# Kernel tuning notes

Hardware: AMD Instinct MI355X
Metric: run time of the kernel (lower is better)

Reference implementation:

```python
import jax, jax.numpy as jnp
import numpy as np

EPS = 1e-05
KEEP_RATIO = 0.7


def setup_inputs() -> dict:
    key = jax.random.key(0)
    ks = jax.random.split(key, 10)
    B, C, L, H = 8, 512, 8192, 128
    return {
        "x": jax.random.normal(ks[0], (B, C, L), dtype=jnp.float32),
        "c": jax.random.normal(ks[1], (B, C, L), dtype=jnp.float32),
        "gw1": jax.random.normal(ks[2], (H, C), dtype=jnp.float32) * 0.05,
        "gb1": jax.random.normal(ks[3], (H,), dtype=jnp.float32) * 0.05,
        "gw2": jax.random.normal(ks[4], (C, H), dtype=jnp.float32) * 0.05,
        "gb2": jax.random.normal(ks[5], (C,), dtype=jnp.float32) * 0.05,
        "mw1": jax.random.normal(ks[6], (H, C), dtype=jnp.float32) * 0.05,
        "mb1": jax.random.normal(ks[7], (H,), dtype=jnp.float32) * 0.05,
        "mw2": jax.random.normal(ks[8], (2 * C, H), dtype=jnp.float32) * 0.05,
        "mb2": jax.random.normal(ks[9], (2 * C,), dtype=jnp.float32) * 0.05,
    }


def reference(x, c, gw1, gb1, gw2, gb2, mw1, mb1, mw2, mb2):
    B, C, L = x.shape
    # per-channel stats over L
    mu_c = jnp.mean(x, axis=2, keepdims=True)                 # [B,C,1]
    var_c = jnp.var(x, axis=2, keepdims=True)                 # ddof=0
    sigma_c = jnp.sqrt(var_c + EPS)
    # per-sample stats over (C,L)
    mu_l = jnp.mean(x, axis=(1, 2), keepdims=True)            # [B,1,1]
    var_l = jnp.var(x, axis=(1, 2), keepdims=True)
    sigma_l = jnp.sqrt(var_l + EPS)
    # gate network on c (1x1 convs == channel matmuls), then mean over L
    h = jax.nn.relu(jnp.einsum('hc,bcl->bhl', gw1, c) + gb1[None, :, None])
    g = jax.nn.sigmoid(jnp.einsum('ch,bhl->bcl', gw2, h) + gb2[None, :, None])
    g_mix = jnp.mean(g, axis=2, keepdims=True)                # [B,C,1]
    mu = g_mix * mu_c + (1.0 - g_mix) * mu_l
    sigma = g_mix * sigma_c + (1.0 - g_mix) * sigma_l
    x_hat = (x - mu) / sigma
    # MLP on pooled condition -> gamma, beta
    cond_pool = jnp.mean(c, axis=2)                           # [B,C]
    hm = jax.nn.relu(jnp.einsum('hc,bc->bh', mw1, cond_pool) + mb1)
    gamma_beta = jnp.einsum('oh,bh->bo', mw2, hm) + mb2       # [B,2C]
    gamma = gamma_beta[:, :C][:, :, None]                     # [B,C,1]
    beta = gamma_beta[:, C:][:, :, None]
    y = (1.0 + gamma) * x_hat + beta
    # top-k channel mask by mean |y| over L
    imp = jnp.mean(jnp.abs(y), axis=2)                        # [B,C]
    k = max(1, int(C * KEEP_RATIO))
    _, idx = jax.lax.top_k(imp, k)                            # [B,k]
    mask = jnp.zeros((B, C), dtype=y.dtype).at[jnp.arange(B)[:, None], idx].set(1.0)
    return y * mask[:, :, None]
```

## Files before the change

kernel.cpp:

```cpp
#include <hip/hip_runtime.h>
#include <hip/hip_bf16.h>
#include <math.h>

#define NB 8
#define NC 512
#define NL 8192
#define NH 128
#define FEPS 1e-5f
#define NKEEP 358

typedef __attribute__((ext_vector_type(8))) short short8;
typedef __attribute__((ext_vector_type(4))) float f32x4;

__device__ __forceinline__ unsigned short f2bf(float x) {
  unsigned u = __float_as_uint(x);
  return (unsigned short)((u + 0x7fffu + ((u >> 16) & 1u)) >> 16);
}
__device__ __forceinline__ unsigned pack2(float a, float b) {
  return (unsigned)f2bf(a) | ((unsigned)f2bf(b) << 16);
}

__global__ __launch_bounds__(256) void k1_xstats(
    const float* __restrict__ x, float* __restrict__ xsum, float* __restrict__ xsumsq,
    const float* __restrict__ gw1, const float* __restrict__ gw2,
    unsigned short* __restrict__ gw1b, unsigned short* __restrict__ gw2b,
    float* __restrict__ csum, float* __restrict__ gsum) {
  const int bc = blockIdx.x;
  const int t = threadIdx.x;
  if (bc < 256) {
    const int i = bc * 256 + t;
    gw1b[i] = f2bf(gw1[i]);
    gw2b[i] = f2bf(gw2[i]);
    if (i < NB * NC) { csum[i] = 0.f; gsum[i] = 0.f; }
  }
  const float4* xp = reinterpret_cast<const float4*>(x + (size_t)bc * NL);
  float s1 = 0.f, s2 = 0.f;
#pragma unroll
  for (int i = 0; i < 8; ++i) {
    float4 v = xp[i * 256 + t];
    s1 += v.x + v.y + v.z + v.w;
    s2 += v.x * v.x + v.y * v.y + v.z * v.z + v.w * v.w;
  }
  for (int off = 32; off; off >>= 1) { s1 += __shfl_down(s1, off); s2 += __shfl_down(s2, off); }
  __shared__ float r1[4], r2[4];
  if ((t & 63) == 0) { r1[t >> 6] = s1; r2[t >> 6] = s2; }
  __syncthreads();
  if (t == 0) {
    xsum[bc]   = r1[0] + r1[1] + r1[2] + r1[3];
    xsumsq[bc] = r2[0] + r2[1] + r2[2] + r2[3];
  }
}

__global__ __launch_bounds__(256, 2) void k2_gate(
    const float* __restrict__ cin,
    const unsigned short* __restrict__ gw1b, const unsigned short* __restrict__ gw2b,
    const float* __restrict__ gb1, const float* __restrict__ gb2,
    float* __restrict__ gsum_g, float* __restrict__ csum_g) {
  __shared__ __align__(16) unsigned AsU[2 * 128 * 36];
  __shared__ __align__(16) unsigned short Hts[4][32][136];
  __shared__ float gsum_s[NC], csum_s[NC], gb2_s[NC];
  __shared__ float gb1_s[NH];

  const int t = threadIdx.x;
  const int lane = t & 63;
  const int w = t >> 6;
  const int r = lane & 15;
  const int kg = lane >> 4;
  const int b = blockIdx.x >> 6;
  const int l0 = (blockIdx.x & 63) * 128;

  const int p = t >> 3;
  const int q = t & 7;

  f32x4 acc0[8], acc1[8];
#pragma unroll
  for (int i = 0; i < 8; ++i) { acc0[i] = (f32x4){0.f,0.f,0.f,0.f}; acc1[i] = (f32x4){0.f,0.f,0.f,0.f}; }

  const float* cbase = cin + (size_t)b * NC * NL + l0;
  const unsigned short* gw1r = gw1b + (size_t)r * NC + kg * 8;

  f32x4 vaA[4], vbA[4], vaB[4], vbB[4];

#define LOADA(dA, dB, kch) { \
    _Pragma("unroll") \
    for (int pass = 0; pass < 4; ++pass) { \
      const float* cp0 = cbase + (size_t)((kch) * 64 + 2 * p) * NL + 32 * pass + 4 * q; \
      dA[pass] = __builtin_nontemporal_load(reinterpret_cast<const f32x4*>(cp0)); \
      dB[pass] = __builtin_nontemporal_load(reinterpret_cast<const f32x4*>(cp0 + NL)); \
    } }

#define WRITEA(sA, sB, kch, bufi) { \
    unsigned* dst = AsU + (bufi) * (128 * 36); \
    float sa = 0.f, sb = 0.f; \
    _Pragma("unroll") \
    for (int pass = 0; pass < 4; ++pass) { \
      const int ll = 32 * pass + 4 * q; \
      sa += sA[pass].x + sA[pass].y + sA[pass].z + sA[pass].w; \
      sb += sB[pass].x + sB[pass].y + sB[pass].z + sB[pass].w; \
      dst[(ll + 0) * 36 + p] = pack2(sA[pass].x, sB[pass].x); \
      dst[(ll + 1) * 36 + p] = pack2(sA[pass].y, sB[pass].y); \
      dst[(ll + 2) * 36 + p] = pack2(sA[pass].z, sB[pass].z); \
      dst[(ll + 3) * 36 + p] = pack2(sA[pass].w, sB[pass].w); \
    } \
    sa += __shfl_xor(sa, 1); sa += __shfl_xor(sa, 2); sa += __shfl_xor(sa, 4); \
    sb += __shfl_xor(sb, 1); sb += __shfl_xor(sb, 2); sb += __shfl_xor(sb, 4); \
    if ((lane & 7) == 0) { \
      atomicAdd(&csum_s[(kch) * 64 + 2 * p],     sa); \
      atomicAdd(&csum_s[(kch) * 64 + 2 * p + 1], sb); \
    } }

  LOADA(vaA, vbA, 0)
  LOADA(vaB, vbB, 1)
  for (int i = t; i < NC; i += 256) { gsum_s[i] = 0.f; csum_s[i] = 0.f; gb2_s[i] = gb2[i]; }
  if (t < NH) gb1_s[t] = gb1[t];
  __syncthreads();
  WRITEA(vaA, vbA, 0, 0)
  asm volatile("s_waitcnt lgkmcnt(0)" ::: "memory");
  __builtin_amdgcn_s_barrier();
  __builtin_amdgcn_sched_barrier(0);

  for (int k = 0; k < 8; ++k) {
    const unsigned* Abuf = AsU + (k & 1) * (128 * 36);
    short8 bfr[16];
#pragma unroll
    for (int ht = 0; ht < 8; ++ht) {
      bfr[2 * ht]     = *reinterpret_cast<const short8*>(gw1r + (size_t)(ht * 16) * NC + k * 64);
      bfr[2 * ht + 1] = *reinterpret_cast<const short8*>(gw1r + (size_t)(ht * 16) * NC + k * 64 + 32);
    }
    short8 a0[2], a1[2];
#pragma unroll
    for (int kk = 0; kk < 2; ++kk) {
      a0[kk] = *reinterpret_cast<const short8*>(&Abuf[(32 * w + r)      * 36 + 16 * kk + 4 * kg]);
      a1[kk] = *reinterpret_cast<const short8*>(&Abuf[(32 * w + 16 + r) * 36 + 16 * kk + 4 * kg]);
    }
    __builtin_amdgcn_sched_barrier(0);
    if (k < 7) {
      if ((k & 1) == 0) { WRITEA(vaB, vbB, k + 1, 1) } else { WRITEA(vaA, vbA, k + 1, 0) }
    }
    __builtin_amdgcn_sched_barrier(0);
    if (k < 6) {
      if ((k & 1) == 0) { LOADA(vaA, vbA, k + 2) } else { LOADA(vaB, vbB, k + 2) }
    }
    __builtin_amdgcn_sched_barrier(0);
#pragma unroll
    for (int kk = 0; kk < 2; ++kk) {
#pragma unroll
      for (int ht = 0; ht < 8; ++ht) {
        acc0[ht] = __builtin_amdgcn_mfma_f32_16x16x32_bf16(a0[kk], bfr[2 * ht + kk], acc0[ht], 0, 0, 0);
        acc1[ht] = __builtin_amdgcn_mfma_f32_16x16x32_bf16(a1[kk], bfr[2 * ht + kk], acc1[ht], 0, 0, 0);
      }
    }
    __builtin_amdgcn_sched_barrier(0);
    asm volatile("s_waitcnt lgkmcnt(0)" ::: "memory");
    __builtin_amdgcn_s_barrier();
    __builtin_amdgcn_sched_barrier(0);
  }

#pragma unroll
  for (int ht = 0; ht < 8; ++ht) {
    const float bias = gb1_s[16 * ht + r];
#pragma unroll
    for (int reg = 0; reg < 4; ++reg) {
      Hts[w][4 * kg + reg][16 * ht + r]      = f2bf(fmaxf(acc0[ht][reg] + bias, 0.f));
      Hts[w][16 + 4 * kg + reg][16 * ht + r] = f2bf(fmaxf(acc1[ht][reg] + bias, 0.f));
    }
  }
  short8 af0[4], af1[4];
#pragma unroll
  for (int kk = 0; kk < 4; ++kk) {
    af0[kk] = *reinterpret_cast<const short8*>(&Hts[w][r][32 * kk + 8 * kg]);
    af1[kk] = *reinterpret_cast<const short8*>(&Hts[w][16 + r][32 * kk + 8 * kg]);
  }

  unsigned short* Bs2 = reinterpret_cast<unsigned short*>(AsU);
  const int crow = lane >> 4;
  const int bs2  = lane & 15;
  short8 bv[4];

#define LOADB2(ccn) { \
    _Pragma("unroll") \
    for (int j = 0; j < 4; ++j) { \
      const int cl = 16 * w + 4 * j + crow; \
      bv[j] = *reinterpret_cast<const short8*>(gw2b + (size_t)((ccn) * 64 + cl) * NH + bs2 * 8); \
    } }
#define WRITEB2(ccn) { \
    unsigned short* dstb = Bs2 + ((ccn) & 1) * 8192; \
    _Pragma("unroll") \
    for (int j = 0; j < 4; ++j) { \
      const int cl = 16 * w + 4 * j + crow; \
      *reinterpret_cast<short8*>(&dstb[cl * 128 + ((bs2 ^ (cl & 7)) * 8)]) = bv[j]; \
    } }

  LOADB2(0)
  WRITEB2(0)
  __syncthreads();
  for (int cc = 0; cc < 8; ++cc) {
    if (cc < 7) LOADB2(cc + 1)
    const unsigned short* Bbuf = Bs2 + (cc & 1) * 8192;
#pragma unroll
    for (int ctt = 0; ctt < 4; ++ctt) {
      f32x4 z0 = (f32x4){0.f,0.f,0.f,0.f}, z1 = (f32x4){0.f,0.f,0.f,0.f};
#pragma unroll
      for (int kk = 0; kk < 4; ++kk) {
        const short8 bf = *reinterpret_cast<const short8*>(
            &Bbuf[(16 * ctt + r) * 128 + (((4 * kk + kg) ^ (r & 7)) * 8)]);
        z0 = __builtin_amdgcn_mfma_f32_16x16x32_bf16(af0[kk], bf, z0, 0, 0, 0);
        z1 = __builtin_amdgcn_mfma_f32_16x16x32_bf16(af1[kk], bf, z1, 0, 0, 0);
      }
      const float bias = gb2_s[cc * 64 + 16 * ctt + r];
      float s = 0.f;
#pragma unroll
      for (int reg = 0; reg < 4; ++reg) {
        s += 1.f / (1.f + __expf(-(z0[reg] + bias)));
        s += 1.f / (1.f + __expf(-(z1[reg] + bias)));
      }
      s += __shfl_xor(s, 16);
      s += __shfl_xor(s, 32);
      if (lane < 16) atomicAdd(&gsum_s[cc * 64 + 16 * ctt + lane], s);
    }
    if (cc < 7) WRITEB2(cc + 1)
    __syncthreads();
  }
  for (int i = t; i < NC; i += 256) {
    atomicAdd(&gsum_g[b * NC + i], gsum_s[i]);
    atomicAdd(&csum_g[b * NC + i], csum_s[i]);
  }
}

__global__ __launch_bounds__(256) void k3_final(
    const float* __restrict__ xsum, const float* __restrict__ xsumsq,
    const float* __restrict__ csum, const float* __restrict__ gsum,
    const float* __restrict__ mw1, const float* __restrict__ mb1,
    const float* __restrict__ mw2, const float* __restrict__ mb2,
    float* __restrict__ a_arr, float* __restrict__ d_arr) {
  __shared__ __align__(16) float cp[NC];
  __shared__ __align__(16) float hm[NH];
  __shared__ float gbv[2 * NC];
  __shared__ double red[8];
  __shared__ float mu_l_s, sig_l_s;
  const int b = blockIdx.x, t = threadIdx.x;

  double s1 = 0.0, s2 = 0.0;
  for (int c = t; c < NC; c += 256) { s1 += (double)xsum[b * NC + c]; s2 += (double)xsumsq[b * NC + c]; }
  for (int off = 32; off; off >>= 1) { s1 += __shfl_down(s1, off); s2 += __shfl_down(s2, off); }
  if ((t & 63) == 0) { red[(t >> 6) * 2] = s1; red[(t >> 6) * 2 + 1] = s2; }
  for (int c = t; c < NC; c += 256) cp[c] = csum[b * NC + c] * (1.f / NL);
  __syncthreads();
  if (t == 0) {
    double S1 = red[0] + red[2] + red[4] + red[6];
    double S2 = red[1] + red[3] + red[5] + red[7];
    double n = (double)NC * NL;
    double mu = S1 / n;
    double var = S2 / n - mu * mu;
    mu_l_s = (float)mu;
    sig_l_s = (float)sqrt(var + (double)FEPS);
  }
  __syncthreads();
  if (t < NH) {
    const float4* row = reinterpret_cast<const float4*>(mw1 + (size_t)t * NC);
    const float4* cpv = reinterpret_cast<const float4*>(cp);
    float acc = mb1[t];
    for (int i = 0; i < NC / 4; ++i) {
      float4 wv = row[i], xv = cpv[i];
      acc += wv.x * xv.x + wv.y * xv.y + wv.z * xv.z + wv.w * xv.w;
    }
    hm[t] = fmaxf(acc, 0.f);
  }
  __syncthreads();
  for (int o = t; o < 2 * NC; o += 256) {
    const float4* row = reinterpret_cast<const float4*>(mw2 + (size_t)o * NH);
    const float4* hv = reinterpret_cast<const float4*>(hm);
    float acc = mb2[o];
    for (int i = 0; i < NH / 4; ++i) {
      float4 wv = row[i], xv = hv[i];
      acc += wv.x * xv.x + wv.y * xv.y + wv.z * xv.z + wv.w * xv.w;
    }
    gbv[o] = acc;
  }
  __syncthreads();
  const float mu_l = mu_l_s, sig_l = sig_l_s;
  for (int c = t; c < NC; c += 256) {
    float gm = gsum[b * NC + c] * (1.f / NL);
    double mu_c = (double)xsum[b * NC + c] / NL;
    double var_c = (double)xsumsq[b * NC + c] / NL - mu_c * mu_c;
    float sig_c = (float)sqrt(var_c + (double)FEPS);
    float mu = gm * (float)mu_c + (1.f - gm) * mu_l;
    float sg = gm * sig_c + (1.f - gm) * sig_l;
    float gamma = gbv[c], beta = gbv[NC + c];
    float A = (1.f + gamma) / sg;
    a_arr[b * NC + c] = A;
    d_arr[b * NC + c] = beta - A * mu;
  }
}

__global__ __launch_bounds__(256) void k4_y(
    const float* __restrict__ x, const float* __restrict__ a_arr,
    const float* __restrict__ d_arr, float* __restrict__ out, float* __restrict__ imp) {
  const int bc = blockIdx.x, t = threadIdx.x;
  const float A = a_arr[bc], D = d_arr[bc];
  const f32x4* xp = reinterpret_cast<const f32x4*>(x + (size_t)bc * NL);
  f32x4* op = reinterpret_cast<f32x4*>(out + (size_t)bc * NL);
  float s = 0.f;
#pragma unroll
  for (int i = 0; i < 8; ++i) {
    f32x4 v = __builtin_nontemporal_load(xp + i * 256 + t);
    f32x4 y;
    y.x = fmaf(A, v.x, D); y.y = fmaf(A, v.y, D);
    y.z = fmaf(A, v.z, D); y.w = fmaf(A, v.w, D);
    s += fabsf(y.x) + fabsf(y.y) + fabsf(y.z) + fabsf(y.w);
    __builtin_nontemporal_store(y, op + i * 256 + t);
  }
  for (int off = 32; off; off >>= 1) s += __shfl_down(s, off);
  __shared__ float rs[4];
  if ((t & 63) == 0) rs[t >> 6] = s;
  __syncthreads();
  if (t == 0) imp[bc] = rs[0] + rs[1] + rs[2] + rs[3];
}

__global__ __launch_bounds__(256) void k5_apply(
    const float* __restrict__ imp, float* __restrict__ out) {
  const int bc = blockIdx.x;
  const int b = bc >> 9;
  const int c = bc & (NC - 1);
  const int t = threadIdx.x;
  const float* row = imp + b * NC;
  const float mine = row[c];
  int cnt = 0;
#pragma unroll
  for (int jj = 0; jj < 2; ++jj) {
    const int j = jj * 256 + t;
    const float o = row[j];
    cnt += (o > mine) || (o == mine && j < c);
  }
  for (int off = 32; off; off >>= 1) cnt += __shfl_down(cnt, off);
  __shared__ int rs[4];
  if ((t & 63) == 0) rs[t >> 6] = cnt;
  __syncthreads();
  const int rank = rs[0] + rs[1] + rs[2] + rs[3];
  if (rank < NKEEP) return;
  f32x4* op = reinterpret_cast<f32x4*>(out + (size_t)bc * NL);
  const f32x4 z = (f32x4){0.f, 0.f, 0.f, 0.f};
#pragma unroll
  for (int i = 0; i < 8; ++i) __builtin_nontemporal_store(z, op + i * 256 + t);
}

extern "C" void kernel_launch(void* const* d_in, const int* in_sizes, int n_in,
                              void* d_out, int out_size, void* d_ws, size_t ws_size,
                              hipStream_t stream) {
  const float* x   = (const float*)d_in[0];
  const float* c   = (const float*)d_in[1];
  const float* gw1 = (const float*)d_in[2];
  const float* gb1 = (const float*)d_in[3];
  const float* gw2 = (const float*)d_in[4];
  const float* gb2 = (const float*)d_in[5];
  const float* mw1 = (const float*)d_in[6];
  const float* mb1 = (const float*)d_in[7];
  const float* mw2 = (const float*)d_in[8];
  const float* mb2 = (const float*)d_in[9];
  float* out = (float*)d_out;
  char* ws = (char*)d_ws;

  unsigned short* gw1b = (unsigned short*)(ws);
  unsigned short* gw2b = (unsigned short*)(ws + 131072);
  float* xsum   = (float*)(ws + 262144);
  float* xsumsq = (float*)(ws + 278528);
  float* csum   = (float*)(ws + 294912);
  float* gsum   = (float*)(ws + 311296);
  float* a_arr  = (float*)(ws + 327680);
  float* d_arr  = (float*)(ws + 344064);
  float* imp    = (float*)(ws + 360448);

  k1_xstats<<<NB * NC, 256, 0, stream>>>(x, xsum, xsumsq, gw1, gw2, gw1b, gw2b, csum, gsum);
  k2_gate<<<NB * (NL / 128), 256, 0, stream>>>(c, gw1b, gw2b, gb1, gb2, gsum, csum);
  k3_final<<<NB, 256, 0, stream>>>(xsum, xsumsq, csum, gsum, mw1, mb1, mw2, mb2, a_arr, d_arr);
  k4_y<<<NB * NC, 256, 0, stream>>>(x, a_arr, d_arr, out, imp);
  k5_apply<<<NB * NC, 256, 0, stream>>>(imp, out);
}
```

Baseline: 170.9 us.

## Merge x-statistics blocks into gate kernel launch to overlap with GEMM work

Weight bf16 conversion and accumulator zeroing move into a small prep kernel. The x-statistics reduction blocks are appended to the gate kernel's grid, so the memory-bound x reads run alongside the compute-heavy gate GEMM blocks in a single launch. The aim is to fill idle bandwidth during the gate phase and remove a serialized kernel boundary. The trade-off is that x-stat blocks inherit the gate kernel's large shared-memory footprint and launch bounds, which may limit how many of them can be resident at once.

```diff
diff --git a/kernel.cpp b/kernel.cpp
--- a/kernel.cpp
+++ b/kernel.cpp
@@ -20,42 +20,44 @@
   return (unsigned)f2bf(a) | ((unsigned)f2bf(b) << 16);
 }
 
-__global__ __launch_bounds__(256) void k1_xstats(
-    const float* __restrict__ x, float* __restrict__ xsum, float* __restrict__ xsumsq,
+__global__ __launch_bounds__(256) void k0_prep(
     const float* __restrict__ gw1, const float* __restrict__ gw2,
     unsigned short* __restrict__ gw1b, unsigned short* __restrict__ gw2b,
     float* __restrict__ csum, float* __restrict__ gsum) {
-  const int bc = blockIdx.x;
-  const int t = threadIdx.x;
-  if (bc < 256) {
-    const int i = bc * 256 + t;
-    gw1b[i] = f2bf(gw1[i]);
-    gw2b[i] = f2bf(gw2[i]);
-    if (i < NB * NC) { csum[i] = 0.f; gsum[i] = 0.f; }
-  }
-  const float4* xp = reinterpret_cast<const float4*>(x + (size_t)bc * NL);
-  float s1 = 0.f, s2 = 0.f;
-#pragma unroll
-  for (int i = 0; i < 8; ++i) {
-    float4 v = xp[i * 256 + t];
-    s1 += v.x + v.y + v.z + v.w;
-    s2 += v.x * v.x + v.y * v.y + v.z * v.z + v.w * v.w;
-  }
-  for (int off = 32; off; off >>= 1) { s1 += __shfl_down(s1, off); s2 += __shfl_down(s2, off); }
-  __shared__ float r1[4], r2[4];
-  if ((t & 63) == 0) { r1[t >> 6] = s1; r2[t >> 6] = s2; }
-  __syncthreads();
-  if (t == 0) {
-    xsum[bc]   = r1[0] + r1[1] + r1[2] + r1[3];
-    xsumsq[bc] = r2[0] + r2[1] + r2[2] + r2[3];
-  }
-}
-
-__global__ __launch_bounds__(256, 2) void k2_gate(
-    const float* __restrict__ cin,
+  int i = blockIdx.x * 256 + threadIdx.x;
+  gw1b[i] = f2bf(gw1[i]);
+  gw2b[i] = f2bf(gw2[i]);
+  if (i < NB * NC) { csum[i] = 0.f; gsum[i] = 0.f; }
+}
+
+__global__ __launch_bounds__(256, 2) void k12_gate_x(
+    const float* __restrict__ cin, const float* __restrict__ x,
     const unsigned short* __restrict__ gw1b, const unsigned short* __restrict__ gw2b,
     const float* __restrict__ gb1, const float* __restrict__ gb2,
-    float* __restrict__ gsum_g, float* __restrict__ csum_g) {
+    float* __restrict__ gsum_g, float* __restrict__ csum_g,
+    float* __restrict__ xsum, float* __restrict__ xsumsq) {
+  if (blockIdx.x >= 512) {
+    const int bc = blockIdx.x - 512;
+    const int t = threadIdx.x;
+    const float4* xp = reinterpret_cast<const float4*>(x + (size_t)bc * NL);
+    float s1 = 0.f, s2 = 0.f;
+#pragma unroll
+    for (int i = 0; i < 8; ++i) {
+      float4 v = xp[i * 256 + t];
+      s1 += v.x + v.y + v.z + v.w;
+      s2 += v.x * v.x + v.y * v.y + v.z * v.z + v.w * v.w;
+    }
+    for (int off = 32; off; off >>= 1) { s1 += __shfl_down(s1, off); s2 += __shfl_down(s2, off); }
+    __shared__ float r1x[4], r2x[4];
+    if ((t & 63) == 0) { r1x[t >> 6] = s1; r2x[t >> 6] = s2; }
+    __syncthreads();
+    if (t == 0) {
+      xsum[bc]   = r1x[0] + r1x[1] + r1x[2] + r1x[3];
+      xsumsq[bc] = r2x[0] + r2x[1] + r2x[2] + r2x[3];
+    }
+    return;
+  }
+
   __shared__ __align__(16) unsigned AsU[2 * 128 * 36];
   __shared__ __align__(16) unsigned short Hts[4][32][136];
   __shared__ float gsum_s[NC], csum_s[NC], gb2_s[NC];
@@ -370,8 +372,9 @@
   float* d_arr  = (float*)(ws + 344064);
   float* imp    = (float*)(ws + 360448);
 
-  k1_xstats<<<NB * NC, 256, 0, stream>>>(x, xsum, xsumsq, gw1, gw2, gw1b, gw2b, csum, gsum);
-  k2_gate<<<NB * (NL / 128), 256, 0, stream>>>(c, gw1b, gw2b, gb1, gb2, gsum, csum);
+  k0_prep<<<256, 256, 0, stream>>>(gw1, gw2, gw1b, gw2b, csum, gsum);
+  k12_gate_x<<<512 + NB * NC, 256, 0, stream>>>(c, x, gw1b, gw2b, gb1, gb2,
+                                                gsum, csum, xsum, xsumsq);
   k3_final<<<NB, 256, 0, stream>>>(xsum, xsumsq, csum, gsum, mw1, mb1, mw2, mb2, a_arr, d_arr);
   k4_y<<<NB * NC, 256, 0, stream>>>(x, a_arr, d_arr, out, imp);
   k5_apply<<<NB * NC, 256, 0, stream>>>(imp, out);
```

Result: faster. 164.9 us (-3.5%).
